# Kernel tuning notes

Hardware: AMD Instinct MI355X
Metric: run time of the kernel (lower is better)

The kernel has to match this reference:

```python
import jax, jax.numpy as jnp
import numpy as np

B, N_IN, K_OUT, C_IN, C_OUT = 32, 2048, 128, 16, 16
NUM_ITERS = 3


def squash_v1(x, axis):
    s2 = (x ** 2).sum(axis, keepdims=True)
    return (jnp.sqrt(s2) / (0.5 + s2)) * x


def setup_inputs() -> dict:
    key = jax.random.key(0)
    k1, k2, k3 = jax.random.split(key, 3)
    x = jax.random.normal(k1, (B, N_IN, C_IN), dtype=jnp.float32)
    y = jax.random.normal(k2, (B, K_OUT), dtype=jnp.float32)  # unused by forward
    labels = jnp.arange(K_OUT, dtype=jnp.int64)
    # xavier-uniform-ish init for W1 [N_in, K_out, out_ch, in_ch] (leading 1 dropped)
    bound = float(np.sqrt(6.0 / (C_IN + C_OUT)))
    W1 = jax.random.uniform(k3, (N_IN, K_OUT, C_OUT, C_IN), dtype=jnp.float32,
                            minval=-bound, maxval=bound)
    return {"x": x, "y": y, "labels": labels, "W1": W1}


def reference(x, y, labels, W1):
    # select output capsules, then u_hat[b,i,k,d] = sum_c W[i,k,d,c] * x[b,i,c]
    W = W1[:, labels]                                   # [N, K, D, C]
    u_hat = jnp.einsum('ikdc,bic->bikd', W, x)          # [B, N, K, D]
    u_sq = squash_v1(u_hat, axis=-1)                    # reused each iteration
    b = jnp.zeros(u_hat.shape[:3], dtype=u_hat.dtype)   # [B, N, K]
    v = None
    for i in range(NUM_ITERS):
        c = jax.nn.softmax(b, axis=2)                   # over output capsules
        c = c / c.sum(axis=1, keepdims=True)            # normalize over input caps
        v = squash_v1(jnp.einsum('bik,bikd->bkd', c, u_hat), axis=-1)  # [B, K, D]
        if i < NUM_ITERS - 1:
            dd = 1.0 - ((u_sq - v[:, None]) ** 2).sum(-1)  # [B, N, K]
            b = b + dd
    poses = v                                           # [B, K, D]
    activations = jnp.sqrt((poses ** 2).sum(-1))        # [B, K]
    return poses, activations
```

## Files before the change

kernel.cpp:

```cpp
#include <hip/hip_runtime.h>


typedef __attribute__((ext_vector_type(8))) short  s16x8;
typedef __attribute__((ext_vector_type(4))) float  f32x4;

#define NSLICE 64

__device__ __forceinline__ unsigned bf16rn(float f) {
    const unsigned u = __builtin_bit_cast(unsigned, f);
    return (u + 0x7fffu + ((u >> 16) & 1u)) >> 16;
}
__device__ __forceinline__ unsigned pack2rn(float a, float b) {
    return bf16rn(a) | (bf16rn(b) << 16);
}
__device__ __forceinline__ unsigned phi(float a, float b) {
    return (__builtin_bit_cast(unsigned, a) >> 16) | (__builtin_bit_cast(unsigned, b) & 0xffff0000u);
}
__device__ __forceinline__ unsigned plo(float a, float b) {
    const float la = a - __builtin_bit_cast(float, __builtin_bit_cast(unsigned, a) & 0xffff0000u);
    const float lb = b - __builtin_bit_cast(float, __builtin_bit_cast(unsigned, b) & 0xffff0000u);
    return pack2rn(la, lb);
}

__device__ __forceinline__ void pack_A(const float* __restrict__ xp, s16x8& A1, s16x8& A2) {
    const float4 x0 = *(const float4*)xp;
    const float4 x1 = *(const float4*)(xp + 4);
    uint4 h, l;
    h.x = phi(x0.x, x0.y); h.y = phi(x0.z, x0.w);
    h.z = phi(x1.x, x1.y); h.w = phi(x1.z, x1.w);
    l.x = plo(x0.x, x0.y); l.y = plo(x0.z, x0.w);
    l.z = plo(x1.x, x1.y); l.w = plo(x1.z, x1.w);
    A1 = __builtin_bit_cast(s16x8, h);
    A2 = __builtin_bit_cast(s16x8, l);
}

__device__ __forceinline__ s16x8 pack_B_f(const float4 w0, const float4 w1, bool sel) {
    const float f[8] = {w0.x, w0.y, w0.z, w0.w, w1.x, w1.y, w1.z, w1.w};
    float t[8];
#pragma unroll
    for (int j = 0; j < 8; ++j) {
        const float hf = __builtin_bit_cast(float, __builtin_bit_cast(unsigned, f[j]) & 0xffff0000u);
        t[j] = sel ? hf : (f[j] - hf);
    }
    uint4 bw;
    bw.x = pack2rn(t[0], t[1]);
    bw.y = pack2rn(t[2], t[3]);
    bw.z = pack2rn(t[4], t[5]);
    bw.w = pack2rn(t[6], t[7]);
    return __builtin_bit_cast(s16x8, bw);
}
__device__ __forceinline__ s16x8 pack_B(const float* __restrict__ wp, bool sel) {
    return pack_B_f(*(const float4*)wp, *(const float4*)(wp + 4), sel);
}

__global__ __launch_bounds__(256) void k_packX(const float* __restrict__ x,
                                               s16x8* __restrict__ xA)
{
    const int wid  = blockIdx.x * 4 + (threadIdx.x >> 6);
    const int lane = threadIdx.x & 63;
    const int i  = wid >> 1, bg = wid & 1;
    const int n  = lane & 15, q = lane >> 4;
    const int oct = (q & 1) * 8;
    s16x8 A1, A2;
    pack_A(x + ((size_t)(bg * 16 + n) * 2048 + i) * 16 + oct, A1, A2);
    s16x8* o = xA + ((size_t)wid * 64 + lane) * 2;
    o[0] = A1;
    o[1] = A2;
}

__global__ __launch_bounds__(256) void k_packWacc(const float* __restrict__ W,
                                                  const s16x8* __restrict__ xA,
                                                  s16x8* __restrict__ Wp,
                                                  float* __restrict__ out_sl)
{
    const int w    = blockIdx.x * 4 + (threadIdx.x >> 6);
    const int lane = threadIdx.x & 63;
    const int n    = lane & 15;
    const int q    = lane >> 4;
    const int oct  = (q & 1) * 8;
    const bool sel = (q < 2);
    const int k0    = (w & 63) * 2;
    const int slice = w >> 6;
    const int i0    = slice * 32;

    const f32x4 zero = {0.f, 0.f, 0.f, 0.f};
    f32x4 acc[2][2];
#pragma unroll
    for (int kp = 0; kp < 2; ++kp)
#pragma unroll
        for (int bg = 0; bg < 2; ++bg) acc[kp][bg] = zero;

    float4 rw0[2], rw1[2];
    s16x8 X1c[2], X2c[2];
    {
        const float* wp_ = W + (size_t)i0 * 32768 + (size_t)k0 * 256 + n * 16 + oct;
        rw0[0] = *(const float4*)wp_;          rw1[0] = *(const float4*)(wp_ + 4);
        rw0[1] = *(const float4*)(wp_ + 256);  rw1[1] = *(const float4*)(wp_ + 260);
        const s16x8* xp = xA + (size_t)i0 * 256 + (size_t)lane * 2;
        X1c[0] = xp[0];   X2c[0] = xp[1];
        X1c[1] = xp[128]; X2c[1] = xp[129];
    }

#pragma unroll 1
    for (int i = i0; i < i0 + 32; ++i) {
        const int in_ = (i + 1 < i0 + 32) ? i + 1 : i;
        float4 nw0[2], nw1[2];
        s16x8 X1n[2], X2n[2];
        {
            const float* wp_ = W + (size_t)in_ * 32768 + (size_t)k0 * 256 + n * 16 + oct;
            nw0[0] = *(const float4*)wp_;          nw1[0] = *(const float4*)(wp_ + 4);
            nw0[1] = *(const float4*)(wp_ + 256);  nw1[1] = *(const float4*)(wp_ + 260);
            const s16x8* xp = xA + (size_t)in_ * 256 + (size_t)lane * 2;
            X1n[0] = xp[0];   X2n[0] = xp[1];
            X1n[1] = xp[128]; X2n[1] = xp[129];
        }
#pragma unroll
        for (int kp = 0; kp < 2; ++kp) {
            const s16x8 Wf = pack_B_f(rw0[kp], rw1[kp], sel);
            Wp[((size_t)i * 128 + (k0 + kp)) * 64 + lane] = Wf;
#pragma unroll
            for (int bg = 0; bg < 2; ++bg) {
                acc[kp][bg] = __builtin_amdgcn_mfma_f32_16x16x32_bf16(Wf, X1c[bg], acc[kp][bg], 0, 0, 0);
                acc[kp][bg] = __builtin_amdgcn_mfma_f32_16x16x32_bf16(Wf, X2c[bg], acc[kp][bg], 0, 0, 0);
            }
        }
#pragma unroll
        for (int kp = 0; kp < 2; ++kp) { rw0[kp] = nw0[kp]; rw1[kp] = nw1[kp]; }
#pragma unroll
        for (int bg = 0; bg < 2; ++bg) { X1c[bg] = X1n[bg]; X2c[bg] = X2n[bg]; }
    }
#pragma unroll
    for (int kp = 0; kp < 2; ++kp)
#pragma unroll
        for (int bg = 0; bg < 2; ++bg)
            *(f32x4*)(out_sl + (((size_t)slice * 32 + bg * 16 + n) * 128 + (k0 + kp)) * 16 + 4 * q)
                = acc[kp][bg];
}

template<bool USE_P, bool PK>
__global__ __launch_bounds__(256) void k_acc(const float* __restrict__ W,
                                             const float* __restrict__ x,
                                             const s16x8* __restrict__ Wp,
                                             const s16x8* __restrict__ xA,
                                             const float* __restrict__ p,
                                             float* __restrict__ out_sl,
                                             float* __restrict__ csl)
{
    const int w    = blockIdx.x * 4 + (threadIdx.x >> 6);
    const int lane = threadIdx.x & 63;
    const int n    = lane & 15;
    const int q    = lane >> 4;
    const int oct  = (q & 1) * 8;
    const bool sel = (q < 2);
    const int k0    = (w & 63) * 2;
    const int slice = w >> 6;
    const int i0    = slice * 32;

    const f32x4 zero = {0.f, 0.f, 0.f, 0.f};
    f32x4 acc[2][2];
    float csacc[2][2];
#pragma unroll
    for (int kp = 0; kp < 2; ++kp)
#pragma unroll
        for (int bg = 0; bg < 2; ++bg) { acc[kp][bg] = zero; csacc[kp][bg] = 0.f; }

    if constexpr (PK) {
        s16x8 X1c[2], X2c[2], Wc[2];
        float pc[2][2];
        {
            const s16x8* xp = xA + (size_t)i0 * 256 + (size_t)lane * 2;
            X1c[0] = xp[0];   X2c[0] = xp[1];
            X1c[1] = xp[128]; X2c[1] = xp[129];
            Wc[0] = Wp[((size_t)i0 * 128 + k0) * 64 + lane];
            Wc[1] = Wp[((size_t)i0 * 128 + k0 + 1) * 64 + lane];
            if (USE_P) {
#pragma unroll
                for (int kp = 0; kp < 2; ++kp)
#pragma unroll
                    for (int bg = 0; bg < 2; ++bg)
                        pc[kp][bg] = p[((size_t)i0 * 128 + k0 + kp) * 32 + bg * 16 + n];
            }
        }
#pragma unroll 1
        for (int i = i0; i < i0 + 32; ++i) {
            const int in_ = (i + 1 < i0 + 32) ? i + 1 : i;
            s16x8 X1n[2], X2n[2], Wn[2];
            float pn[2][2];
            {
                const s16x8* xp = xA + (size_t)in_ * 256 + (size_t)lane * 2;
                X1n[0] = xp[0];   X2n[0] = xp[1];
                X1n[1] = xp[128]; X2n[1] = xp[129];
                Wn[0] = Wp[((size_t)in_ * 128 + k0) * 64 + lane];
                Wn[1] = Wp[((size_t)in_ * 128 + k0 + 1) * 64 + lane];
                if (USE_P) {
#pragma unroll
                    for (int kp = 0; kp < 2; ++kp)
#pragma unroll
                        for (int bg = 0; bg < 2; ++bg)
                            pn[kp][bg] = p[((size_t)in_ * 128 + k0 + kp) * 32 + bg * 16 + n];
                }
            }
#pragma unroll
            for (int kp = 0; kp < 2; ++kp) {
#pragma unroll
                for (int bg = 0; bg < 2; ++bg) {
                    if (USE_P) {
                        f32x4 u = __builtin_amdgcn_mfma_f32_16x16x32_bf16(Wc[kp], X1c[bg], zero, 0, 0, 0);
                        u       = __builtin_amdgcn_mfma_f32_16x16x32_bf16(Wc[kp], X2c[bg], u,    0, 0, 0);
                        const float pv = pc[kp][bg];
                        acc[kp][bg].x = fmaf(pv, u.x, acc[kp][bg].x);
                        acc[kp][bg].y = fmaf(pv, u.y, acc[kp][bg].y);
                        acc[kp][bg].z = fmaf(pv, u.z, acc[kp][bg].z);
                        acc[kp][bg].w = fmaf(pv, u.w, acc[kp][bg].w);
                        csacc[kp][bg] += pv;
                    } else {
                        acc[kp][bg] = __builtin_amdgcn_mfma_f32_16x16x32_bf16(Wc[kp], X1c[bg], acc[kp][bg], 0, 0, 0);
                        acc[kp][bg] = __builtin_amdgcn_mfma_f32_16x16x32_bf16(Wc[kp], X2c[bg], acc[kp][bg], 0, 0, 0);
                    }
                }
            }
#pragma unroll
            for (int kp = 0; kp < 2; ++kp) Wc[kp] = Wn[kp];
#pragma unroll
            for (int bg = 0; bg < 2; ++bg) { X1c[bg] = X1n[bg]; X2c[bg] = X2n[bg]; }
            if (USE_P) {
#pragma unroll
                for (int kp = 0; kp < 2; ++kp)
#pragma unroll
                    for (int bg = 0; bg < 2; ++bg) pc[kp][bg] = pn[kp][bg];
            }
        }
    } else {
#pragma unroll 1
        for (int i = i0; i < i0 + 32; ++i) {
            s16x8 X1[2], X2[2];
#pragma unroll
            for (int bg = 0; bg < 2; ++bg)
                pack_A(x + ((size_t)(bg * 16 + n) * 2048 + i) * 16 + oct, X1[bg], X2[bg]);
#pragma unroll
            for (int kp = 0; kp < 2; ++kp) {
                const int k = k0 + kp;
                const s16x8 Wf = pack_B(W + (size_t)i * 32768 + (size_t)k * 256 + n * 16 + oct, sel);
#pragma unroll
                for (int bg = 0; bg < 2; ++bg) {
                    if (USE_P) {
                        f32x4 u = __builtin_amdgcn_mfma_f32_16x16x32_bf16(Wf, X1[bg], zero, 0, 0, 0);
                        u       = __builtin_amdgcn_mfma_f32_16x16x32_bf16(Wf, X2[bg], u,    0, 0, 0);
                        const float pv = p[((size_t)i * 128 + k) * 32 + bg * 16 + n];
                        acc[kp][bg].x = fmaf(pv, u.x, acc[kp][bg].x);
                        acc[kp][bg].y = fmaf(pv, u.y, acc[kp][bg].y);
                        acc[kp][bg].z = fmaf(pv, u.z, acc[kp][bg].z);
                        acc[kp][bg].w = fmaf(pv, u.w, acc[kp][bg].w);
                        csacc[kp][bg] += pv;
                    } else {
                        acc[kp][bg] = __builtin_amdgcn_mfma_f32_16x16x32_bf16(Wf, X1[bg], acc[kp][bg], 0, 0, 0);
                        acc[kp][bg] = __builtin_amdgcn_mfma_f32_16x16x32_bf16(Wf, X2[bg], acc[kp][bg], 0, 0, 0);
                    }
                }
            }
        }
    }
#pragma unroll
    for (int kp = 0; kp < 2; ++kp)
#pragma unroll
        for (int bg = 0; bg < 2; ++bg)
            *(f32x4*)(out_sl + (((size_t)slice * 32 + bg * 16 + n) * 128 + (k0 + kp)) * 16 + 4 * q)
                = acc[kp][bg];
    if (USE_P && lane < 16) {
#pragma unroll
        for (int kp = 0; kp < 2; ++kp)
#pragma unroll
            for (int bg = 0; bg < 2; ++bg)
                csl[((size_t)slice * 128 + (k0 + kp)) * 32 + bg * 16 + n] = csacc[kp][bg];
    }
}

template<bool PK>
__global__ __launch_bounds__(512) void k_logits(const float* __restrict__ W,
                                                const float* __restrict__ x,
                                                const s16x8* __restrict__ Wp,
                                                const s16x8* __restrict__ xA,
                                                const float* __restrict__ Vq,
                                                const float* __restrict__ Nt,
                                                const float T,
                                                float* __restrict__ pbuf)
{
    __shared__ __align__(16) float e_s[8][16][32];
    __shared__ __align__(16) float den_s[8][32];
    __shared__ float denom_s[32];
    const int tid  = threadIdx.x;
    const int wv   = tid >> 6, lane = tid & 63;
    const int n    = lane & 15, q = lane >> 4;
    const int oct  = (q & 1) * 8;
    const bool sel = (q < 2);
    const f32x4 zero = {0.f, 0.f, 0.f, 0.f};

    const int pk = tid >> 2;
    const int pb = (tid & 3) * 8;

    const int i0 = blockIdx.x * 4;
#pragma unroll 1
    for (int ii = 0; ii < 4; ++ii) {
        const int i = i0 + ii;
        s16x8 X1[2], X2[2];
        if constexpr (PK) {
            const s16x8* xp = xA + (size_t)i * 256 + (size_t)lane * 2;
            X1[0] = xp[0];   X2[0] = xp[1];
            X1[1] = xp[128]; X2[1] = xp[129];
        } else {
#pragma unroll
            for (int bg = 0; bg < 2; ++bg)
                pack_A(x + ((size_t)(bg * 16 + n) * 2048 + i) * 16 + oct, X1[bg], X2[bg]);
        }

        float den0 = 0.f, den1 = 0.f;
        s16x8 Wf;
        if constexpr (PK) Wf = Wp[((size_t)i * 128 + wv * 16) * 64 + lane];
#pragma unroll
        for (int kp = 0; kp < 16; ++kp) {
            const int k = wv * 16 + kp;
            if constexpr (!PK) {
                Wf = pack_B(W + (size_t)i * 32768 + (size_t)k * 256 + n * 16 + oct, sel);
            }
            s16x8 Wfn;
            if constexpr (PK) {
                const int kn = (kp < 15) ? k + 1 : k;
                Wfn = Wp[((size_t)i * 128 + kn) * 64 + lane];
            }
            float ebg[2];
#pragma unroll
            for (int bg = 0; bg < 2; ++bg) {
                f32x4 u = __builtin_amdgcn_mfma_f32_16x16x32_bf16(Wf, X1[bg], zero, 0, 0, 0);
                u       = __builtin_amdgcn_mfma_f32_16x16x32_bf16(Wf, X2[bg], u,    0, 0, 0);
                const float4 Vv = *(const float4*)(Vq + (((size_t)k * 4 + q) * 32 + bg * 16 + n) * 4);
                float s2 = u.x * u.x;
                s2 = fmaf(u.y, u.y, s2);
                s2 = fmaf(u.z, u.z, s2);
                s2 = fmaf(u.w, u.w, s2);
                float dt = u.x * Vv.x;
                dt = fmaf(u.y, Vv.y, dt);
                dt = fmaf(u.z, Vv.z, dt);
                dt = fmaf(u.w, Vv.w, dt);
                s2 += __shfl_xor(s2, 16, 64);
                s2 += __shfl_xor(s2, 32, 64);
                dt += __shfl_xor(dt, 16, 64);
                dt += __shfl_xor(dt, 32, 64);
                const float Nr  = Nt[(size_t)k * 32 + bg * 16 + n];
                const float inv = 1.0f / (0.5f + s2);
                const float scl = sqrtf(s2) * inv;
                const float fq  = s2 * s2 * inv * inv;
                const float e   = __expf(T * (1.0f - fq) + 2.0f * scl * dt - Nr);
                if (bg == 0) den0 += e; else den1 += e;
                ebg[bg] = e;
            }
            if (lane < 16) {
                e_s[wv][kp][n]      = ebg[0];
                e_s[wv][kp][16 + n] = ebg[1];
            }
            if constexpr (PK) Wf = Wfn;
        }
        if (lane < 16) {
            den_s[wv][n]      = den0;
            den_s[wv][16 + n] = den1;
        }
        __syncthreads();
        if (tid < 32) {
            float s = 0.f;
#pragma unroll
            for (int w2 = 0; w2 < 8; ++w2) s += den_s[w2][tid];
            denom_s[tid] = s;
        }
        __syncthreads();
        {
            const float4 e0 = *(const float4*)&e_s[pk >> 4][pk & 15][pb];
            const float4 e1 = *(const float4*)&e_s[pk >> 4][pk & 15][pb + 4];
            const float4 d0 = *(const float4*)&denom_s[pb];
            const float4 d1 = *(const float4*)&denom_s[pb + 4];
            float4 p0, p1;
            p0.x = e0.x / d0.x; p0.y = e0.y / d0.y; p0.z = e0.z / d0.z; p0.w = e0.w / d0.w;
            p1.x = e1.x / d1.x; p1.y = e1.y / d1.y; p1.z = e1.z / d1.z; p1.w = e1.w / d1.w;
            *(float4*)(pbuf + ((size_t)i * 128 + pk) * 32 + pb)     = p0;
            *(float4*)(pbuf + ((size_t)i * 128 + pk) * 32 + pb + 4) = p1;
        }
        __syncthreads();
    }
}

__global__ __launch_bounds__(256) void k_fin(const float* __restrict__ raw_sl,
                                             const float* __restrict__ csl,
                                             const float* __restrict__ Vq_prev,
                                             const float* __restrict__ Nt_prev,
                                             float* __restrict__ Vq_out,
                                             float* __restrict__ Nt_out,
                                             float* __restrict__ out,
                                             const int mode)
{
    const int tid = threadIdx.x;
    const int t   = blockIdx.x * 16 + (tid >> 4);
    const int d   = tid & 15;
    const int b   = t >> 7, k = t & 127;
    float s = 0.f, cs = 0.f;
    if (mode == 0) {
#pragma unroll 4
        for (int sl = 0; sl < NSLICE; ++sl) s += raw_sl[(size_t)sl * 65536 + (size_t)t * 16 + d];
    } else {
#pragma unroll 4
        for (int sl = 0; sl < NSLICE; ++sl) {
            s  += raw_sl[(size_t)sl * 65536 + (size_t)t * 16 + d];
            cs += csl[(size_t)sl * 4096 + k * 32 + b];
        }
    }
    const float invcs = (mode == 0) ? (1.0f / 2048.0f) : 1.0f / cs;
    const float v = s * invcs;
    float s2 = v * v;
#pragma unroll
    for (int m = 1; m < 16; m <<= 1) s2 += __shfl_xor(s2, m, 64);
    const float inv = 1.0f / (0.5f + s2);
    const float scl = sqrtf(s2) * inv;
    const size_t vidx = (((size_t)k * 4 + (d >> 2)) * 32 + b) * 4 + (d & 3);
    if (mode == 0) {
        Vq_out[vidx] = scl * v;
        if (d == 0) Nt_out[(size_t)k * 32 + b] = s2 * scl * scl;
    } else if (mode == 1) {
        Vq_out[vidx] = Vq_prev[vidx] + scl * v;
        if (d == 0) Nt_out[(size_t)k * 32 + b] = Nt_prev[(size_t)k * 32 + b] + s2 * scl * scl;
    } else {
        out[(size_t)t * 16 + d] = scl * v;
        if (d == 0) out[65536 + t] = s2 * inv;
    }
}

extern "C" void kernel_launch(void* const* d_in, const int* in_sizes, int n_in,
                              void* d_out, int out_size, void* d_ws, size_t ws_size,
                              hipStream_t stream)
{
    const float* x = (const float*)d_in[0];
    const float* W = (const float*)d_in[3];

    float* ws    = (float*)d_ws;
    float* Vbt0  = ws;
    float* VSbt  = ws + 65536;
    float* N1t   = ws + 131072;
    float* N2t   = ws + 135168;
    float* csl   = ws + 139264;
    float* pbuf  = ws + 401408;
    float* slces = ws + 8790016;

    s16x8* Wp = (s16x8*)(ws + 12984320);
    s16x8* xA = (s16x8*)((short*)Wp + (size_t)134217728);
    const size_t needed = (size_t)12984320 * 4
                        + (size_t)134217728 * 2
                        + (size_t)8388608 * 2;
    const bool pk = (ws_size >= needed);

    if (pk) {
        k_packX<<<1024, 256, 0, stream>>>(x, xA);
        k_packWacc<<<1024, 256, 0, stream>>>(W, xA, Wp, slces);
        k_fin<<<256, 256, 0, stream>>>(slces, nullptr, nullptr, nullptr, Vbt0, N1t, nullptr, 0);
        k_logits<true><<<512, 512, 0, stream>>>(W, x, Wp, xA, Vbt0, N1t, 1.0f, pbuf);
        k_acc<true, true><<<1024, 256, 0, stream>>>(W, x, Wp, xA, pbuf, slces, csl);
        k_fin<<<256, 256, 0, stream>>>(slces, csl, Vbt0, N1t, VSbt, N2t, nullptr, 1);
        k_logits<true><<<512, 512, 0, stream>>>(W, x, Wp, xA, VSbt, N2t, 2.0f, pbuf);
        k_acc<true, true><<<1024, 256, 0, stream>>>(W, x, Wp, xA, pbuf, slces, csl);
        k_fin<<<256, 256, 0, stream>>>(slces, csl, nullptr, nullptr, nullptr, nullptr, (float*)d_out, 2);
    } else {
        k_acc<false, false><<<1024, 256, 0, stream>>>(W, x, nullptr, nullptr, nullptr, slces, nullptr);
        k_fin<<<256, 256, 0, stream>>>(slces, nullptr, nullptr, nullptr, Vbt0, N1t, nullptr, 0);
        k_logits<false><<<512, 512, 0, stream>>>(W, x, nullptr, nullptr, Vbt0, N1t, 1.0f, pbuf);
        k_acc<true, false><<<1024, 256, 0, stream>>>(W, x, nullptr, nullptr, pbuf, slces, csl);
        k_fin<<<256, 256, 0, stream>>>(slces, csl, Vbt0, N1t, VSbt, N2t, nullptr, 1);
        k_logits<false><<<512, 512, 0, stream>>>(W, x, nullptr, nullptr, VSbt, N2t, 2.0f, pbuf);
        k_acc<true, false><<<1024, 256, 0, stream>>>(W, x, nullptr, nullptr, pbuf, slces, csl);
        k_fin<<<256, 256, 0, stream>>>(slces, csl, nullptr, nullptr, nullptr, nullptr, (float*)d_out, 2);
    }
}
```

Baseline: 780.9 us.

## Fuse routing logits, softmax and weighted accumulation into one per-iteration kernel

Replaces the separate logits kernel (which wrote normalized coupling coefficients to a global buffer) and the accumulation kernel with a single k_iter kernel. Each 1024-thread block handles 8 input capsules across all 128 output capsules, computes exp-logits, reduces the softmax denominator in shared memory, then recomputes u_hat via MFMA and accumulates the p-weighted sum. This removes the pbuf global write/read round trip and one launch per iteration. In exchange u_hat is computed twice per iteration, there are two block barriers per input capsule, and the number of slices rises to 256, so the finalize reduction reads more partial sums.

```diff
diff --git a/kernel.cpp b/kernel.cpp
--- a/kernel.cpp
+++ b/kernel.cpp
@@ -3,8 +3,6 @@
 
 typedef __attribute__((ext_vector_type(8))) short  s16x8;
 typedef __attribute__((ext_vector_type(4))) float  f32x4;
-
-#define NSLICE 64
 
 __device__ __forceinline__ unsigned bf16rn(float f) {
     const unsigned u = __builtin_bit_cast(unsigned, f);
@@ -137,14 +135,121 @@
                 = acc[kp][bg];
 }
 
-template<bool USE_P, bool PK>
-__global__ __launch_bounds__(256) void k_acc(const float* __restrict__ W,
-                                             const float* __restrict__ x,
-                                             const s16x8* __restrict__ Wp,
-                                             const s16x8* __restrict__ xA,
-                                             const float* __restrict__ p,
-                                             float* __restrict__ out_sl,
-                                             float* __restrict__ csl)
+__global__ __launch_bounds__(1024) void k_iter(const s16x8* __restrict__ Wp,
+                                               const s16x8* __restrict__ xA,
+                                               const float* __restrict__ Vq,
+                                               const float* __restrict__ Nt,
+                                               const float T,
+                                               float* __restrict__ out_sl,
+                                               float* __restrict__ csl)
+{
+    __shared__ __align__(16) float e_s[16][8][32];
+    __shared__ __align__(16) float den_s[16][32];
+    __shared__ float denom_s[32];
+    const int tid  = threadIdx.x;
+    const int wv   = tid >> 6, lane = tid & 63;
+    const int n    = lane & 15, q = lane >> 4;
+    const int c     = blockIdx.x;
+    const int i0    = c * 8;
+    const int kbase = wv * 8;
+    const f32x4 zero = {0.f, 0.f, 0.f, 0.f};
+
+    f32x4 acc[8][2];
+    float cs0[2][2];
+#pragma unroll
+    for (int kp = 0; kp < 8; ++kp)
+#pragma unroll
+        for (int bg = 0; bg < 2; ++bg) acc[kp][bg] = zero;
+    cs0[0][0] = cs0[0][1] = cs0[1][0] = cs0[1][1] = 0.f;
+
+#pragma unroll 1
+    for (int ii = 0; ii < 8; ++ii) {
+        const int i = i0 + ii;
+        const s16x8* xp = xA + (size_t)i * 256 + (size_t)lane * 2;
+        const s16x8 X1[2] = {xp[0], xp[128]};
+        const s16x8 X2[2] = {xp[1], xp[129]};
+        const s16x8* wrow = Wp + ((size_t)i * 128 + kbase) * 64 + lane;
+
+        float den0 = 0.f, den1 = 0.f;
+#pragma unroll 2
+        for (int kp = 0; kp < 8; ++kp) {
+            const int k = kbase + kp;
+            const s16x8 Wf = wrow[(size_t)kp * 64];
+#pragma unroll
+            for (int bg = 0; bg < 2; ++bg) {
+                f32x4 u = __builtin_amdgcn_mfma_f32_16x16x32_bf16(Wf, X1[bg], zero, 0, 0, 0);
+                u       = __builtin_amdgcn_mfma_f32_16x16x32_bf16(Wf, X2[bg], u,    0, 0, 0);
+                const float4 Vv = *(const float4*)(Vq + (((size_t)k * 4 + q) * 32 + bg * 16 + n) * 4);
+                float s2 = u.x * u.x;
+                s2 = fmaf(u.y, u.y, s2);
+                s2 = fmaf(u.z, u.z, s2);
+                s2 = fmaf(u.w, u.w, s2);
+                float dt = u.x * Vv.x;
+                dt = fmaf(u.y, Vv.y, dt);
+                dt = fmaf(u.z, Vv.z, dt);
+                dt = fmaf(u.w, Vv.w, dt);
+                s2 += __shfl_xor(s2, 16, 64);
+                s2 += __shfl_xor(s2, 32, 64);
+                dt += __shfl_xor(dt, 16, 64);
+                dt += __shfl_xor(dt, 32, 64);
+                const float Nr  = Nt[(size_t)k * 32 + bg * 16 + n];
+                const float inv = 1.0f / (0.5f + s2);
+                const float scl = sqrtf(s2) * inv;
+                const float fq  = s2 * s2 * inv * inv;
+                const float e   = __expf(T * (1.0f - fq) + 2.0f * scl * dt - Nr);
+                if (bg == 0) den0 += e; else den1 += e;
+                if (lane < 16) e_s[wv][kp][bg * 16 + n] = e;
+            }
+        }
+        if (lane < 16) {
+            den_s[wv][n]      = den0;
+            den_s[wv][16 + n] = den1;
+        }
+        __syncthreads();
+        if (tid < 32) {
+            float s = 0.f;
+#pragma unroll
+            for (int w2 = 0; w2 < 16; ++w2) s += den_s[w2][tid];
+            denom_s[tid] = s;
+        }
+        __syncthreads();
+        const float inv0 = 1.0f / denom_s[n];
+        const float inv1 = 1.0f / denom_s[16 + n];
+#pragma unroll 2
+        for (int kp = 0; kp < 8; ++kp) {
+            const s16x8 Wf = wrow[(size_t)kp * 64];
+#pragma unroll
+            for (int bg = 0; bg < 2; ++bg) {
+                f32x4 u = __builtin_amdgcn_mfma_f32_16x16x32_bf16(Wf, X1[bg], zero, 0, 0, 0);
+                u       = __builtin_amdgcn_mfma_f32_16x16x32_bf16(Wf, X2[bg], u,    0, 0, 0);
+                const float p = e_s[wv][kp][bg * 16 + n] * (bg == 0 ? inv0 : inv1);
+                acc[kp][bg].x = fmaf(p, u.x, acc[kp][bg].x);
+                acc[kp][bg].y = fmaf(p, u.y, acc[kp][bg].y);
+                acc[kp][bg].z = fmaf(p, u.z, acc[kp][bg].z);
+                acc[kp][bg].w = fmaf(p, u.w, acc[kp][bg].w);
+                cs0[kp & 1][bg] += ((kp >> 1) == q) ? p : 0.f;
+            }
+        }
+    }
+#pragma unroll
+    for (int kp = 0; kp < 8; ++kp)
+#pragma unroll
+        for (int bg = 0; bg < 2; ++bg)
+            *(f32x4*)(out_sl + (((size_t)c * 32 + bg * 16 + n) * 128 + (kbase + kp)) * 16 + 4 * q)
+                = acc[kp][bg];
+#pragma unroll
+    for (int j = 0; j < 2; ++j)
+#pragma unroll
+        for (int bg = 0; bg < 2; ++bg)
+            csl[((size_t)c * 128 + kbase + 2 * q + j) * 32 + bg * 16 + n] = cs0[j][bg];
+}
+
+template<bool USE_P>
+__global__ __launch_bounds__(256) void k_acc_fb(const float* __restrict__ W,
+                                                const float* __restrict__ x,
+                                                const float* __restrict__ p,
+                                                float* __restrict__ out_sl,
+                                                float* __restrict__ csl)
 {
     const int w    = blockIdx.x * 4 + (threadIdx.x >> 6);
     const int lane = threadIdx.x & 63;
@@ -164,98 +269,30 @@
 #pragma unroll
         for (int bg = 0; bg < 2; ++bg) { acc[kp][bg] = zero; csacc[kp][bg] = 0.f; }
 
-    if constexpr (PK) {
-        s16x8 X1c[2], X2c[2], Wc[2];
-        float pc[2][2];
-        {
-            const s16x8* xp = xA + (size_t)i0 * 256 + (size_t)lane * 2;
-            X1c[0] = xp[0];   X2c[0] = xp[1];
-            X1c[1] = xp[128]; X2c[1] = xp[129];
-            Wc[0] = Wp[((size_t)i0 * 128 + k0) * 64 + lane];
-            Wc[1] = Wp[((size_t)i0 * 128 + k0 + 1) * 64 + lane];
-            if (USE_P) {
-#pragma unroll
-                for (int kp = 0; kp < 2; ++kp)
-#pragma unroll
-                    for (int bg = 0; bg < 2; ++bg)
-                        pc[kp][bg] = p[((size_t)i0 * 128 + k0 + kp) * 32 + bg * 16 + n];
-            }
-        }
 #pragma unroll 1
-        for (int i = i0; i < i0 + 32; ++i) {
-            const int in_ = (i + 1 < i0 + 32) ? i + 1 : i;
-            s16x8 X1n[2], X2n[2], Wn[2];
-            float pn[2][2];
-            {
-                const s16x8* xp = xA + (size_t)in_ * 256 + (size_t)lane * 2;
-                X1n[0] = xp[0];   X2n[0] = xp[1];
-                X1n[1] = xp[128]; X2n[1] = xp[129];
-                Wn[0] = Wp[((size_t)in_ * 128 + k0) * 64 + lane];
-                Wn[1] = Wp[((size_t)in_ * 128 + k0 + 1) * 64 + lane];
+    for (int i = i0; i < i0 + 32; ++i) {
+        s16x8 X1[2], X2[2];
+#pragma unroll
+        for (int bg = 0; bg < 2; ++bg)
+            pack_A(x + ((size_t)(bg * 16 + n) * 2048 + i) * 16 + oct, X1[bg], X2[bg]);
+#pragma unroll
+        for (int kp = 0; kp < 2; ++kp) {
+            const int k = k0 + kp;
+            const s16x8 Wf = pack_B(W + (size_t)i * 32768 + (size_t)k * 256 + n * 16 + oct, sel);
+#pragma unroll
+            for (int bg = 0; bg < 2; ++bg) {
                 if (USE_P) {
-#pragma unroll
-                    for (int kp = 0; kp < 2; ++kp)
-#pragma unroll
-                        for (int bg = 0; bg < 2; ++bg)
-                            pn[kp][bg] = p[((size_t)in_ * 128 + k0 + kp) * 32 + bg * 16 + n];
-                }
-            }
-#pragma unroll
-            for (int kp = 0; kp < 2; ++kp) {
-#pragma unroll
-                for (int bg = 0; bg < 2; ++bg) {
-                    if (USE_P) {
-                        f32x4 u = __builtin_amdgcn_mfma_f32_16x16x32_bf16(Wc[kp], X1c[bg], zero, 0, 0, 0);
-                        u       = __builtin_amdgcn_mfma_f32_16x16x32_bf16(Wc[kp], X2c[bg], u,    0, 0, 0);
-                        const float pv = pc[kp][bg];
-                        acc[kp][bg].x = fmaf(pv, u.x, acc[kp][bg].x);
-                        acc[kp][bg].y = fmaf(pv, u.y, acc[kp][bg].y);
-                        acc[kp][bg].z = fmaf(pv, u.z, acc[kp][bg].z);
-                        acc[kp][bg].w = fmaf(pv, u.w, acc[kp][bg].w);
-                        csacc[kp][bg] += pv;
-                    } else {
-                        acc[kp][bg] = __builtin_amdgcn_mfma_f32_16x16x32_bf16(Wc[kp], X1c[bg], acc[kp][bg], 0, 0, 0);
-                        acc[kp][bg] = __builtin_amdgcn_mfma_f32_16x16x32_bf16(Wc[kp], X2c[bg], acc[kp][bg], 0, 0, 0);
-                    }
-                }
-            }
-#pragma unroll
-            for (int kp = 0; kp < 2; ++kp) Wc[kp] = Wn[kp];
-#pragma unroll
-            for (int bg = 0; bg < 2; ++bg) { X1c[bg] = X1n[bg]; X2c[bg] = X2n[bg]; }
-            if (USE_P) {
-#pragma unroll
-                for (int kp = 0; kp < 2; ++kp)
-#pragma unroll
-                    for (int bg = 0; bg < 2; ++bg) pc[kp][bg] = pn[kp][bg];
-            }
-        }
-    } else {
-#pragma unroll 1
-        for (int i = i0; i < i0 + 32; ++i) {
-            s16x8 X1[2], X2[2];
-#pragma unroll
-            for (int bg = 0; bg < 2; ++bg)
-                pack_A(x + ((size_t)(bg * 16 + n) * 2048 + i) * 16 + oct, X1[bg], X2[bg]);
-#pragma unroll
-            for (int kp = 0; kp < 2; ++kp) {
-                const int k = k0 + kp;
-                const s16x8 Wf = pack_B(W + (size_t)i * 32768 + (size_t)k * 256 + n * 16 + oct, sel);
-#pragma unroll
-                for (int bg = 0; bg < 2; ++bg) {
-                    if (USE_P) {
-                        f32x4 u = __builtin_amdgcn_mfma_f32_16x16x32_bf16(Wf, X1[bg], zero, 0, 0, 0);
-                        u       = __builtin_amdgcn_mfma_f32_16x16x32_bf16(Wf, X2[bg], u,    0, 0, 0);
-                        const float pv = p[((size_t)i * 128 + k) * 32 + bg * 16 + n];
-                        acc[kp][bg].x = fmaf(pv, u.x, acc[kp][bg].x);
-                        acc[kp][bg].y = fmaf(pv, u.y, acc[kp][bg].y);
-                        acc[kp][bg].z = fmaf(pv, u.z, acc[kp][bg].z);
-                        acc[kp][bg].w = fmaf(pv, u.w, acc[kp][bg].w);
-                        csacc[kp][bg] += pv;
-                    } else {
-                        acc[kp][bg] = __builtin_amdgcn_mfma_f32_16x16x32_bf16(Wf, X1[bg], acc[kp][bg], 0, 0, 0);
-                        acc[kp][bg] = __builtin_amdgcn_mfma_f32_16x16x32_bf16(Wf, X2[bg], acc[kp][bg], 0, 0, 0);
-                    }
+                    f32x4 u = __builtin_amdgcn_mfma_f32_16x16x32_bf16(Wf, X1[bg], zero, 0, 0, 0);
+                    u       = __builtin_amdgcn_mfma_f32_16x16x32_bf16(Wf, X2[bg], u,    0, 0, 0);
+                    const float pv = p[((size_t)i * 128 + k) * 32 + bg * 16 + n];
+                    acc[kp][bg].x = fmaf(pv, u.x, acc[kp][bg].x);
+                    acc[kp][bg].y = fmaf(pv, u.y, acc[kp][bg].y);
+                    acc[kp][bg].z = fmaf(pv, u.z, acc[kp][bg].z);
+                    acc[kp][bg].w = fmaf(pv, u.w, acc[kp][bg].w);
+                    csacc[kp][bg] += pv;
+                } else {
+                    acc[kp][bg] = __builtin_amdgcn_mfma_f32_16x16x32_bf16(Wf, X1[bg], acc[kp][bg], 0, 0, 0);
+                    acc[kp][bg] = __builtin_amdgcn_mfma_f32_16x16x32_bf16(Wf, X2[bg], acc[kp][bg], 0, 0, 0);
                 }
             }
         }
@@ -275,15 +312,12 @@
     }
 }
 
-template<bool PK>
-__global__ __launch_bounds__(512) void k_logits(const float* __restrict__ W,
-                                                const float* __restrict__ x,
-                                                const s16x8* __restrict__ Wp,
-                                                const s16x8* __restrict__ xA,
-                                                const float* __restrict__ Vq,
-                                                const float* __restrict__ Nt,
-                                                const float T,
-                                                float* __restrict__ pbuf)
+__global__ __launch_bounds__(512) void k_logits_fb(const float* __restrict__ W,
+                                                   const float* __restrict__ x,
+                                                   const float* __restrict__ Vq,
+                                                   const float* __restrict__ Nt,
+                                                   const float T,
+                                                   float* __restrict__ pbuf)
 {
     __shared__ __align__(16) float e_s[8][16][32];
     __shared__ __align__(16) float den_s[8][32];
@@ -294,7 +328,6 @@
     const int oct  = (q & 1) * 8;
     const bool sel = (q < 2);
     const f32x4 zero = {0.f, 0.f, 0.f, 0.f};
-
     const int pk = tid >> 2;
     const int pb = (tid & 3) * 8;
 
@@ -303,30 +336,15 @@
     for (int ii = 0; ii < 4; ++ii) {
         const int i = i0 + ii;
         s16x8 X1[2], X2[2];
-        if constexpr (PK) {
-            const s16x8* xp = xA + (size_t)i * 256 + (size_t)lane * 2;
-            X1[0] = xp[0];   X2[0] = xp[1];
-            X1[1] = xp[128]; X2[1] = xp[129];
-        } else {
-#pragma unroll
-            for (int bg = 0; bg < 2; ++bg)
-                pack_A(x + ((size_t)(bg * 16 + n) * 2048 + i) * 16 + oct, X1[bg], X2[bg]);
-        }
+#pragma unroll
+        for (int bg = 0; bg < 2; ++bg)
+            pack_A(x + ((size_t)(bg * 16 + n) * 2048 + i) * 16 + oct, X1[bg], X2[bg]);
 
         float den0 = 0.f, den1 = 0.f;
-        s16x8 Wf;
-        if constexpr (PK) Wf = Wp[((size_t)i * 128 + wv * 16) * 64 + lane];
 #pragma unroll
         for (int kp = 0; kp < 16; ++kp) {
             const int k = wv * 16 + kp;
-            if constexpr (!PK) {
-                Wf = pack_B(W + (size_t)i * 32768 + (size_t)k * 256 + n * 16 + oct, sel);
-            }
-            s16x8 Wfn;
-            if constexpr (PK) {
-                const int kn = (kp < 15) ? k + 1 : k;
-                Wfn = Wp[((size_t)i * 128 + kn) * 64 + lane];
-            }
+            const s16x8 Wf = pack_B(W + (size_t)i * 32768 + (size_t)k * 256 + n * 16 + oct, sel);
             float ebg[2];
 #pragma unroll
             for (int bg = 0; bg < 2; ++bg) {
@@ -357,7 +375,6 @@
                 e_s[wv][kp][n]      = ebg[0];
                 e_s[wv][kp][16 + n] = ebg[1];
             }
-            if constexpr (PK) Wf = Wfn;
         }
         if (lane < 16) {
             den_s[wv][n]      = den0;
@@ -393,7 +410,8 @@
                                              float* __restrict__ Vq_out,
                                              float* __restrict__ Nt_out,
                                              float* __restrict__ out,
-                                             const int mode)
+                                             const int mode,
+                                             const int nslice)
 {
     const int tid = threadIdx.x;
     const int t   = blockIdx.x * 16 + (tid >> 4);
@@ -402,10 +420,10 @@
     float s = 0.f, cs = 0.f;
     if (mode == 0) {
 #pragma unroll 4
-        for (int sl = 0; sl < NSLICE; ++sl) s += raw_sl[(size_t)sl * 65536 + (size_t)t * 16 + d];
+        for (int sl = 0; sl < nslice; ++sl) s += raw_sl[(size_t)sl * 65536 + (size_t)t * 16 + d];
     } else {
 #pragma unroll 4
-        for (int sl = 0; sl < NSLICE; ++sl) {
+        for (int sl = 0; sl < nslice; ++sl) {
             s  += raw_sl[(size_t)sl * 65536 + (size_t)t * 16 + d];
             cs += csl[(size_t)sl * 4096 + k * 32 + b];
         }
@@ -443,12 +461,11 @@
     float* N1t   = ws + 131072;
     float* N2t   = ws + 135168;
     float* csl   = ws + 139264;
-    float* pbuf  = ws + 401408;
-    float* slces = ws + 8790016;
-
-    s16x8* Wp = (s16x8*)(ws + 12984320);
+    float* slces = ws + 1187840;
+
+    s16x8* Wp = (s16x8*)(ws + 17965056);
     s16x8* xA = (s16x8*)((short*)Wp + (size_t)134217728);
-    const size_t needed = (size_t)12984320 * 4
+    const size_t needed = (size_t)17965056 * 4
                         + (size_t)134217728 * 2
                         + (size_t)8388608 * 2;
     const bool pk = (ws_size >= needed);
@@ -456,21 +473,20 @@
     if (pk) {
         k_packX<<<1024, 256, 0, stream>>>(x, xA);
         k_packWacc<<<1024, 256, 0, stream>>>(W, xA, Wp, slces);
-        k_fin<<<256, 256, 0, stream>>>(slces, nullptr, nullptr, nullptr, Vbt0, N1t, nullptr, 0);
-        k_logits<true><<<512, 512, 0, stream>>>(W, x, Wp, xA, Vbt0, N1t, 1.0f, pbuf);
-        k_acc<true, true><<<1024, 256, 0, stream>>>(W, x, Wp, xA, pbuf, slces, csl);
-        k_fin<<<256, 256, 0, stream>>>(slces, csl, Vbt0, N1t, VSbt, N2t, nullptr, 1);
-        k_logits<true><<<512, 512, 0, stream>>>(W, x, Wp, xA, VSbt, N2t, 2.0f, pbuf);
-        k_acc<true, true><<<1024, 256, 0, stream>>>(W, x, Wp, xA, pbuf, slces, csl);
-        k_fin<<<256, 256, 0, stream>>>(slces, csl, nullptr, nullptr, nullptr, nullptr, (float*)d_out, 2);
+        k_fin<<<256, 256, 0, stream>>>(slces, nullptr, nullptr, nullptr, Vbt0, N1t, nullptr, 0, 64);
+        k_iter<<<256, 1024, 0, stream>>>(Wp, xA, Vbt0, N1t, 1.0f, slces, csl);
+        k_fin<<<256, 256, 0, stream>>>(slces, csl, Vbt0, N1t, VSbt, N2t, nullptr, 1, 256);
+        k_iter<<<256, 1024, 0, stream>>>(Wp, xA, VSbt, N2t, 2.0f, slces, csl);
+        k_fin<<<256, 256, 0, stream>>>(slces, csl, nullptr, nullptr, nullptr, nullptr, (float*)d_out, 2, 256);
     } else {
-        k_acc<false, false><<<1024, 256, 0, stream>>>(W, x, nullptr, nullptr, nullptr, slces, nullptr);
-        k_fin<<<256, 256, 0, stream>>>(slces, nullptr, nullptr, nullptr, Vbt0, N1t, nullptr, 0);
-        k_logits<false><<<512, 512, 0, stream>>>(W, x, nullptr, nullptr, Vbt0, N1t, 1.0f, pbuf);
-        k_acc<true, false><<<1024, 256, 0, stream>>>(W, x, nullptr, nullptr, pbuf, slces, csl);
-        k_fin<<<256, 256, 0, stream>>>(slces, csl, Vbt0, N1t, VSbt, N2t, nullptr, 1);
-        k_logits<false><<<512, 512, 0, stream>>>(W, x, nullptr, nullptr, VSbt, N2t, 2.0f, pbuf);
-        k_acc<true, false><<<1024, 256, 0, stream>>>(W, x, nullptr, nullptr, pbuf, slces, csl);
-        k_fin<<<256, 256, 0, stream>>>(slces, csl, nullptr, nullptr, nullptr, nullptr, (float*)d_out, 2);
-    }
-}
+        float* pbuf = (float*)Wp;
+        k_acc_fb<false><<<1024, 256, 0, stream>>>(W, x, nullptr, slces, nullptr);
+        k_fin<<<256, 256, 0, stream>>>(slces, nullptr, nullptr, nullptr, Vbt0, N1t, nullptr, 0, 64);
+        k_logits_fb<<<512, 512, 0, stream>>>(W, x, Vbt0, N1t, 1.0f, pbuf);
+        k_acc_fb<true><<<1024, 256, 0, stream>>>(W, x, pbuf, slces, csl);
+        k_fin<<<256, 256, 0, stream>>>(slces, csl, Vbt0, N1t, VSbt, N2t, nullptr, 1, 64);
+        k_logits_fb<<<512, 512, 0, stream>>>(W, x, VSbt, N2t, 2.0f, pbuf);
+        k_acc_fb<true><<<1024, 256, 0, stream>>>(W, x, pbuf, slces, csl);
+        k_fin<<<256, 256, 0, stream>>>(slces, csl, nullptr, nullptr, nullptr, nullptr, (float*)d_out, 2, 64);
+    }
+}
```

Measured after the change: 1.255 ms. 60.7% more time.
